# Kernel tuning notes

Hardware: AMD Instinct MI355X
Metric: run time of the kernel (lower is better)

## Reference

```python
import jax, jax.numpy as jnp
import numpy as np

N = 100000      # nodes
E = 1000000     # edges
H_DIM = 124     # node embedding dim
CLS_DIM = 4     # node class-logit dim (H_DIM + CLS_DIM = in_features = 128)
POLAR_DIM = 2   # edge_pred_features
HIDDEN = 256
OUT = 2
LN_EPS = 1e-5


def setup_inputs() -> dict:
    key = jax.random.key(0)
    ks = jax.random.split(key, 10)
    in_dim = 2 * (H_DIM + CLS_DIM) + POLAR_DIM  # 258
    return {
        "h": jax.random.normal(ks[0], (N, H_DIM), dtype=jnp.float32),
        "cls": jax.random.normal(ks[1], (N, CLS_DIM), dtype=jnp.float32),
        "polar": jax.random.normal(ks[2], (E, POLAR_DIM), dtype=jnp.float32),
        "src": jax.random.randint(ks[3], (E,), 0, N, dtype=jnp.int64),
        "dst": jax.random.randint(ks[4], (E,), 0, N, dtype=jnp.int64),
        # parameters (PyTorch Linear default-ish init scale)
        "W1": jax.random.normal(ks[5], (in_dim, HIDDEN), dtype=jnp.float32) * (1.0 / np.sqrt(in_dim)),
        "b1": jnp.zeros((HIDDEN,), dtype=jnp.float32),
        "gamma": jnp.ones((HIDDEN,), dtype=jnp.float32),
        "beta": jnp.zeros((HIDDEN,), dtype=jnp.float32),
        "W2": jax.random.normal(ks[6], (HIDDEN, OUT), dtype=jnp.float32) * (1.0 / np.sqrt(HIDDEN)),
        "b2": jnp.zeros((OUT,), dtype=jnp.float32),
    }


def reference(h, cls, polar, src, dst, W1, b1, gamma, beta, W2, b2):
    # softmax over class logits per node (same math as softmax on gathered
    # edge copies, but computed once per node)
    cls_sm = jax.nn.softmax(cls, axis=1)                  # [N, CLS_DIM]
    # gather src/dst node features along edges
    x = jnp.concatenate(
        [h[src], cls_sm[src], polar, h[dst], cls_sm[dst]], axis=1
    )                                                     # [E, 258]
    z = x @ W1 + b1                                        # [E, HIDDEN]
    # LayerNorm
    mu = jnp.mean(z, axis=-1, keepdims=True)
    var = jnp.mean(jnp.square(z - mu), axis=-1, keepdims=True)
    z = (z - mu) * jax.lax.rsqrt(var + LN_EPS) * gamma + beta
    z = jax.nn.relu(z)
    # dropout is identity in eval mode
    score = z @ W2 + b2                                    # [E, OUT]
    return score
```

## Files before the change

### kernel.cpp

```cpp
#include <hip/hip_runtime.h>
#include <hip/hip_bf16.h>

#define NN 100000
#define EE 1000000
#define H_DIM 124
#define PCOLS 512
#define LDK 136
#define CW 132

typedef float f32x4 __attribute__((ext_vector_type(4)));
typedef short bf16x8 __attribute__((ext_vector_type(8)));
typedef _Float16 h2 __attribute__((ext_vector_type(2)));

__device__ __forceinline__ unsigned short f2bf(float f) {
    unsigned int x = __float_as_uint(f);
    unsigned int r = (x + 0x7FFFu + ((x >> 16) & 1u)) >> 16;
    return (unsigned short)r;
}
__device__ __forceinline__ unsigned int pk2bf(float a, float b) {
    return (unsigned int)f2bf(a) | ((unsigned int)f2bf(b) << 16);
}
__device__ __forceinline__ unsigned int pk2h(float a, float b) {
    h2 v = (h2){(_Float16)a, (_Float16)b};
    return __builtin_bit_cast(unsigned int, v);
}

__device__ __forceinline__ float fdot2(h2 a, h2 b, float c) {
#if __has_builtin(__builtin_amdgcn_fdot2)
    return __builtin_amdgcn_fdot2(a, b, c, false);
#else
    return c + (float)a[0] * (float)b[0] + (float)a[1] * (float)b[1];
#endif
}

#if __has_builtin(__builtin_amdgcn_update_dpp)
template <int CTRL>
__device__ __forceinline__ float dpp_add(float x) {
    int xi = __builtin_bit_cast(int, x);
    int t = __builtin_amdgcn_update_dpp(xi, xi, CTRL, 0xF, 0xF, false);
    return x + __builtin_bit_cast(float, t);
}
__device__ __forceinline__ float reduce16(float x) {
    x = dpp_add<0x128>(x);
    x = dpp_add<0x124>(x);
    x = dpp_add<0x122>(x);
    x = dpp_add<0x121>(x);
    return x;
}
#else
__device__ __forceinline__ float reduce16(float x) {
    x += __shfl_xor(x, 8); x += __shfl_xor(x, 4);
    x += __shfl_xor(x, 2); x += __shfl_xor(x, 1);
    return x;
}
#endif

struct alignas(16) H8 { h2 p[4]; };

__global__ __launch_bounds__(256) void build_w1t_ct(const float* __restrict__ W1,
                                                    const float* __restrict__ gamma,
                                                    const float* __restrict__ beta,
                                                    const float* __restrict__ W2,
                                                    unsigned short* __restrict__ W1T,
                                                    uint4* __restrict__ CT) {
    if (blockIdx.x < 256) {
        int t2 = blockIdx.x * 256 + threadIdx.x;
        int j = t2 >> 7, k = t2 & 127;
        int row = (j < 256) ? k : (130 + k);
        int col = (j < 256) ? j : (j - 256);
        W1T[t2] = f2bf(W1[row * 256 + col]);
    } else {
        int t = threadIdx.x;
        if (t < 192) {
            int slot = t % 12, il = t / 12;
            int a = slot >> 1, k = slot & 1;
            int j0 = il * 16 + k * 8;
            float v[8];
            #pragma unroll
            for (int i = 0; i < 8; ++i) {
                int j = j0 + i;
                v[i] = (a == 0) ? W1[128 * 256 + j]
                     : (a == 1) ? W1[129 * 256 + j]
                     : (a == 2) ? gamma[j]
                     : (a == 3) ? beta[j]
                     : (a == 4) ? W2[2 * j]
                     :            W2[2 * j + 1];
            }
            CT[t] = make_uint4(pk2h(v[0], v[1]), pk2h(v[2], v[3]),
                               pk2h(v[4], v[5]), pk2h(v[6], v[7]));
        }
    }
}

__global__ __launch_bounds__(256) void p_gemm(const float* __restrict__ h,
                                              const float* __restrict__ cls,
                                              const unsigned short* __restrict__ W1T,
                                              const float* __restrict__ b1,
                                              _Float16* __restrict__ P) {
    __shared__ alignas(16) unsigned short As[64 * LDK];
    __shared__ alignas(16) unsigned short Bs[128 * LDK];
    float* Cs = (float*)&Bs[0];
    const int m0 = blockIdx.x * 64;
    const int t = threadIdx.x;

    #pragma unroll
    for (int it = 0; it < 4; ++it) {
        int chunk = t + it * 256;
        int r = chunk >> 4, c8 = chunk & 15;
        int row = m0 + r;
        unsigned int w0 = 0, w1 = 0, w2 = 0, w3 = 0;
        if (row < NN) {
            if (c8 < 15) {
                const float* hp = h + (size_t)row * H_DIM + c8 * 8;
                float4 v0 = *(const float4*)(hp);
                float4 v1 = *(const float4*)(hp + 4);
                w0 = pk2bf(v0.x, v0.y); w1 = pk2bf(v0.z, v0.w);
                w2 = pk2bf(v1.x, v1.y); w3 = pk2bf(v1.z, v1.w);
            } else {
                float4 v0 = *(const float4*)(h + (size_t)row * H_DIM + 120);
                float4 c = *(const float4*)(cls + (size_t)row * 4);
                float m = fmaxf(fmaxf(c.x, c.y), fmaxf(c.z, c.w));
                float e0 = __expf(c.x - m), e1 = __expf(c.y - m);
                float e2 = __expf(c.z - m), e3 = __expf(c.w - m);
                float inv = 1.0f / (e0 + e1 + e2 + e3);
                w0 = pk2bf(v0.x, v0.y); w1 = pk2bf(v0.z, v0.w);
                w2 = pk2bf(e0 * inv, e1 * inv); w3 = pk2bf(e2 * inv, e3 * inv);
            }
        }
        *(uint4*)(&As[r * LDK + c8 * 8]) = make_uint4(w0, w1, w2, w3);
    }
    __syncthreads();

    const int wave = t >> 6, lane = t & 63;
    const int wm = wave & 1, wn = wave >> 1;
    const int lm = lane & 15, quad = lane >> 4;

    bf16x8 afrag[4][2];
    #pragma unroll
    for (int s = 0; s < 4; ++s) {
        int k0 = s * 32 + quad * 8;
        #pragma unroll
        for (int mt = 0; mt < 2; ++mt)
            afrag[s][mt] = *(const bf16x8*)(&As[(wm * 32 + mt * 16 + lm) * LDK + k0]);
    }

    for (int cchunk = 0; cchunk < 4; ++cchunk) {
        const int n0 = cchunk * 128;
        if (cchunk) __syncthreads();
        #pragma unroll
        for (int it = 0; it < 8; ++it) {
            int chunk = t + it * 256;
            int r = chunk >> 4, c = chunk & 15;
            float4 v = *(const float4*)(W1T + (n0 + r) * 128 + c * 8);
            *(float4*)(&Bs[r * LDK + c * 8]) = v;
        }
        __syncthreads();

        f32x4 acc[2][4];
        #pragma unroll
        for (int mt = 0; mt < 2; ++mt)
            #pragma unroll
            for (int nt = 0; nt < 4; ++nt)
                acc[mt][nt] = (f32x4){0.f, 0.f, 0.f, 0.f};

        #pragma unroll
        for (int s = 0; s < 4; ++s) {
            int k0 = s * 32 + quad * 8;
            bf16x8 b[4];
            #pragma unroll
            for (int nt = 0; nt < 4; ++nt)
                b[nt] = *(const bf16x8*)(&Bs[(wn * 64 + nt * 16 + lm) * LDK + k0]);
            #pragma unroll
            for (int mt = 0; mt < 2; ++mt)
                #pragma unroll
                for (int nt = 0; nt < 4; ++nt)
                    acc[mt][nt] = __builtin_amdgcn_mfma_f32_16x16x32_bf16(afrag[s][mt], b[nt], acc[mt][nt], 0, 0, 0);
        }
        __syncthreads();

        #pragma unroll
        for (int mt = 0; mt < 2; ++mt)
            #pragma unroll
            for (int nt = 0; nt < 4; ++nt) {
                int col = wn * 64 + nt * 16 + lm;
                int rb  = wm * 32 + mt * 16 + quad * 4;
                #pragma unroll
                for (int r = 0; r < 4; ++r)
                    Cs[(rb + r) * CW + col] = acc[mt][nt][r];
            }
        __syncthreads();

        #pragma unroll
        for (int it = 0; it < 4; ++it) {
            int chunk = t + it * 256;
            int r = chunk >> 4, c8 = chunk & 15;
            float4 a = *(const float4*)(Cs + r * CW + c8 * 8);
            float4 b = *(const float4*)(Cs + r * CW + c8 * 8 + 4);
            if (n0 >= 256) {
                int cb = n0 + c8 * 8 - 256;
                float4 ba = *(const float4*)(b1 + cb);
                float4 bb = *(const float4*)(b1 + cb + 4);
                a.x += ba.x; a.y += ba.y; a.z += ba.z; a.w += ba.w;
                b.x += bb.x; b.y += bb.y; b.z += bb.z; b.w += bb.w;
            }
            uint4 o = make_uint4(pk2h(a.x, a.y), pk2h(a.z, a.w),
                                 pk2h(b.x, b.y), pk2h(b.z, b.w));
            int row = m0 + r;
            if (row < NN)
                *(uint4*)(P + (size_t)row * PCOLS + n0 + c8 * 8) = o;
        }
    }
}

#define K3_BLOCKS 4096
#define K3_WAVES  (K3_BLOCKS * 4)
#define K3_STRIDE (K3_WAVES * 4)
#define K3_ROUNDS 16

struct EIdx { int s, d; float q0, q1; };

__global__ __launch_bounds__(256) void edge_kernel(const _Float16* __restrict__ P,
                                                   const int* __restrict__ src,
                                                   const int* __restrict__ dst,
                                                   const float* __restrict__ polar,
                                                   const uint4* __restrict__ CT,
                                                   const float* __restrict__ b2,
                                                   float* __restrict__ out) {
    const int lane = threadIdx.x & 63;
    const int il   = lane & 15;
    const int g    = lane >> 4;
    const int wid  = blockIdx.x * 4 + (threadIdx.x >> 6);
    const char* Pb = (const char*)P;
    const int e0 = wid * 4 + g;

    uint4 cq[12];
    #pragma unroll
    for (int i = 0; i < 12; ++i) cq[i] = CT[il * 12 + i];
    h2 w0c[8], w1c[8], gc[8], bc[8], w2ac[8], w2bc[8];
    {
        const h2* ch = (const h2*)cq;
        #pragma unroll
        for (int p = 0; p < 8; ++p) {
            w0c[p]  = ch[p];      w1c[p]  = ch[8 + p];
            gc[p]   = ch[16 + p]; bc[p]   = ch[24 + p];
            w2ac[p] = ch[32 + p]; w2bc[p] = ch[40 + p];
        }
    }
    const float b20 = b2[0], b21 = b2[1];
    const h2 onep  = (h2){(_Float16)1.0f, (_Float16)1.0f};
    const h2 zerop = (h2){(_Float16)0.0f, (_Float16)0.0f};

    const unsigned boff_s = (unsigned)(il * 32);
    const unsigned boff_d = (unsigned)(512 + il * 32);

    EIdx I[4];
    H8 buf[3][4];

    #define LOAD_IDX(slot, r)                                                  \
    {                                                                          \
        int eg = e0 + (r) * K3_STRIDE;                                         \
        int ec = (eg < EE) ? eg : 0;                                           \
        I[slot].s = src[ec]; I[slot].d = dst[ec];                              \
        float2 q = *(const float2*)(polar + 2 * ec);                           \
        I[slot].q0 = q.x; I[slot].q1 = q.y;                                    \
    }

    #define LOAD_P(bslot, islot)                                               \
    {                                                                          \
        unsigned os = (unsigned)I[islot].s * 1024u + boff_s;                   \
        unsigned od = (unsigned)I[islot].d * 1024u + boff_d;                   \
        buf[bslot][0] = *(const H8*)(Pb + os);                                 \
        buf[bslot][1] = *(const H8*)(Pb + os + 16);                            \
        buf[bslot][2] = *(const H8*)(Pb + od);                                 \
        buf[bslot][3] = *(const H8*)(Pb + od + 16);                            \
    }

    LOAD_IDX(0, 0) LOAD_IDX(1, 1) LOAD_IDX(2, 2) LOAD_IDX(3, 3)
    LOAD_P(0, 0) LOAD_P(1, 1) LOAD_P(2, 2)

    #define EDGE_COMPUTE(Abuf, q0v, q1v, eg)                                   \
    {                                                                          \
        h2 p0 = (h2){(_Float16)(q0v), (_Float16)(q0v)};                        \
        h2 p1 = (h2){(_Float16)(q1v), (_Float16)(q1v)};                        \
        h2 z[8];                                                               \
        float sum = 0.f, ss = 0.f;                                             \
        _Pragma("unroll")                                                      \
        for (int p = 0; p < 8; ++p) {                                          \
            h2 pv = ((p < 4) ? (Abuf)[0].p[p] : (Abuf)[1].p[p - 4])            \
                  + ((p < 4) ? (Abuf)[2].p[p] : (Abuf)[3].p[p - 4]);           \
            h2 c = w0c[p] * p0 + w1c[p] * p1;                                  \
            z[p] = pv + c;                                                     \
            sum = fdot2(z[p], onep, sum);                                      \
            ss  = fdot2(z[p], z[p], ss);                                       \
        }                                                                      \
        sum = reduce16(sum); ss = reduce16(ss);                                \
        float mu   = sum * (1.0f / 256.0f);                                    \
        float var  = ss * (1.0f / 256.0f) - mu * mu;                           \
        float rstd = rsqrtf(var + 1e-5f);                                      \
        float nmur = -mu * rstd;                                               \
        h2 rsh  = (h2){(_Float16)rstd, (_Float16)rstd};                        \
        h2 nmh  = (h2){(_Float16)nmur, (_Float16)nmur};                        \
        float o0 = 0.f, o1 = 0.f;                                              \
        _Pragma("unroll")                                                      \
        for (int p = 0; p < 8; ++p) {                                          \
            h2 tt = z[p] * rsh + nmh;                                          \
            h2 u = tt * gc[p] + bc[p];                                         \
            u = __builtin_elementwise_max(u, zerop);                           \
            o0 = fdot2(u, w2ac[p], o0);                                        \
            o1 = fdot2(u, w2bc[p], o1);                                        \
        }                                                                      \
        o0 = reduce16(o0); o1 = reduce16(o1);                                  \
        if (il == 0 && (eg) < EE)                                              \
            *(float2*)(out + 2 * (eg)) = make_float2(o0 + b20, o1 + b21);      \
    }

    #pragma unroll
    for (int r = 0; r < K3_ROUNDS; ++r) {
        const int bi = r % 3, ii = r % 4;
        EDGE_COMPUTE(buf[bi], I[ii].q0, I[ii].q1, e0 + r * K3_STRIDE);
        if (r + 4 < K3_ROUNDS) {
            LOAD_IDX(ii, r + 4)
        }
        if (r + 3 < K3_ROUNDS) {
            LOAD_P(bi, (r + 3) % 4)
        }
    }
    #undef EDGE_COMPUTE
    #undef LOAD_P
    #undef LOAD_IDX
}

extern "C" void kernel_launch(void* const* d_in, const int* in_sizes, int n_in,
                              void* d_out, int out_size, void* d_ws, size_t ws_size,
                              hipStream_t stream) {
    const float* h     = (const float*)d_in[0];
    const float* cls   = (const float*)d_in[1];
    const float* polar = (const float*)d_in[2];
    const int*   src   = (const int*)d_in[3];
    const int*   dst   = (const int*)d_in[4];
    const float* W1    = (const float*)d_in[5];
    const float* b1    = (const float*)d_in[6];
    const float* gamma = (const float*)d_in[7];
    const float* beta  = (const float*)d_in[8];
    const float* W2    = (const float*)d_in[9];
    const float* b2    = (const float*)d_in[10];
    float* out = (float*)d_out;

    char* ws = (char*)d_ws;
    _Float16*       P   = (_Float16*)ws;
    unsigned short* W1T = (unsigned short*)(ws + 102400000);
    uint4*          CT  = (uint4*)(ws + 102531072);

    build_w1t_ct<<<257, 256, 0, stream>>>(W1, gamma, beta, W2, W1T, CT);
    p_gemm<<<1563, 256, 0, stream>>>(h, cls, W1T, b1, P);
    edge_kernel<<<K3_BLOCKS, 256, 0, stream>>>(P, src, dst, polar, CT, b2, out);
}
```

Baseline: 288.1 us.

## Deepen edge gather pipeline to four buffers and split index/polar prefetch

The edge kernel now keeps four P-row gather buffers in flight instead of three, and prefetches src/dst indices eight rounds ahead. The polar loads get their own prefetch slot. The round loop becomes a rolled outer loop over a 4-way unrolled inner body with fixed buffer slots, and the bounds guard is kept only on the final round. The LayerNorm sum is reworked so the mean no longer goes through a dot with ones. This trades more VGPR pressure and some redundant clamped loads past the last round for more memory-level parallelism on the random gathers.

After: 288.0 us. About the same (-0.0%).

```diff
diff --git a/kernel.cpp b/kernel.cpp
--- a/kernel.cpp
+++ b/kernel.cpp
@@ -217,8 +217,6 @@
 #define K3_STRIDE (K3_WAVES * 4)
 #define K3_ROUNDS 16
 
-struct EIdx { int s, d; float q0, q1; };
-
 __global__ __launch_bounds__(256) void edge_kernel(const _Float16* __restrict__ P,
                                                    const int* __restrict__ src,
                                                    const int* __restrict__ dst,
@@ -247,50 +245,55 @@
         }
     }
     const float b20 = b2[0], b21 = b2[1];
-    const h2 onep  = (h2){(_Float16)1.0f, (_Float16)1.0f};
     const h2 zerop = (h2){(_Float16)0.0f, (_Float16)0.0f};
 
     const unsigned boff_s = (unsigned)(il * 32);
     const unsigned boff_d = (unsigned)(512 + il * 32);
 
-    EIdx I[4];
-    H8 buf[3][4];
+    int   Is[4], Id[4];
+    float q[4][2];
+    H8 buf[4][4];
 
     #define LOAD_IDX(slot, r)                                                  \
     {                                                                          \
         int eg = e0 + (r) * K3_STRIDE;                                         \
         int ec = (eg < EE) ? eg : 0;                                           \
-        I[slot].s = src[ec]; I[slot].d = dst[ec];                              \
-        float2 q = *(const float2*)(polar + 2 * ec);                           \
-        I[slot].q0 = q.x; I[slot].q1 = q.y;                                    \
-    }
-
-    #define LOAD_P(bslot, islot)                                               \
+        Is[slot] = src[ec]; Id[slot] = dst[ec];                                \
+    }
+    #define LOAD_Q(slot, r)                                                    \
     {                                                                          \
-        unsigned os = (unsigned)I[islot].s * 1024u + boff_s;                   \
-        unsigned od = (unsigned)I[islot].d * 1024u + boff_d;                   \
-        buf[bslot][0] = *(const H8*)(Pb + os);                                 \
-        buf[bslot][1] = *(const H8*)(Pb + os + 16);                            \
-        buf[bslot][2] = *(const H8*)(Pb + od);                                 \
-        buf[bslot][3] = *(const H8*)(Pb + od + 16);                            \
+        int eg = e0 + (r) * K3_STRIDE;                                         \
+        int ec = (eg < EE) ? eg : 0;                                           \
+        float2 qq = *(const float2*)(polar + 2 * ec);                          \
+        q[slot][0] = qq.x; q[slot][1] = qq.y;                                  \
+    }
+    #define LOAD_P(slot)                                                       \
+    {                                                                          \
+        unsigned os = (unsigned)Is[slot] * 1024u + boff_s;                     \
+        unsigned od = (unsigned)Id[slot] * 1024u + boff_d;                     \
+        buf[slot][0] = *(const H8*)(Pb + os);                                  \
+        buf[slot][1] = *(const H8*)(Pb + os + 16);                             \
+        buf[slot][2] = *(const H8*)(Pb + od);                                  \
+        buf[slot][3] = *(const H8*)(Pb + od + 16);                             \
     }
 
     LOAD_IDX(0, 0) LOAD_IDX(1, 1) LOAD_IDX(2, 2) LOAD_IDX(3, 3)
-    LOAD_P(0, 0) LOAD_P(1, 1) LOAD_P(2, 2)
-
-    #define EDGE_COMPUTE(Abuf, q0v, q1v, eg)                                   \
+    LOAD_Q(0, 0) LOAD_Q(1, 1) LOAD_Q(2, 2) LOAD_Q(3, 3)
+    LOAD_P(0) LOAD_P(1) LOAD_P(2) LOAD_P(3)
+    LOAD_IDX(0, 4) LOAD_IDX(1, 5) LOAD_IDX(2, 6) LOAD_IDX(3, 7)
+
+    #define EDGE_COMPUTE(slot, eg, GUARD)                                      \
     {                                                                          \
-        h2 p0 = (h2){(_Float16)(q0v), (_Float16)(q0v)};                        \
-        h2 p1 = (h2){(_Float16)(q1v), (_Float16)(q1v)};                        \
+        h2 p0 = (h2){(_Float16)q[slot][0], (_Float16)q[slot][0]};              \
+        h2 p1 = (h2){(_Float16)q[slot][1], (_Float16)q[slot][1]};              \
         h2 z[8];                                                               \
         float sum = 0.f, ss = 0.f;                                             \
         _Pragma("unroll")                                                      \
         for (int p = 0; p < 8; ++p) {                                          \
-            h2 pv = ((p < 4) ? (Abuf)[0].p[p] : (Abuf)[1].p[p - 4])            \
-                  + ((p < 4) ? (Abuf)[2].p[p] : (Abuf)[3].p[p - 4]);           \
-            h2 c = w0c[p] * p0 + w1c[p] * p1;                                  \
-            z[p] = pv + c;                                                     \
-            sum = fdot2(z[p], onep, sum);                                      \
+            h2 pv = ((p < 4) ? buf[slot][0].p[p] : buf[slot][1].p[p - 4])      \
+                  + ((p < 4) ? buf[slot][2].p[p] : buf[slot][3].p[p - 4]);     \
+            z[p] = w0c[p] * p0 + (w1c[p] * p1 + pv);                           \
+            sum += (float)z[p][0] + (float)z[p][1];                            \
             ss  = fdot2(z[p], z[p], ss);                                       \
         }                                                                      \
         sum = reduce16(sum); ss = reduce16(ss);                                \
@@ -310,23 +313,28 @@
             o1 = fdot2(u, w2bc[p], o1);                                        \
         }                                                                      \
         o0 = reduce16(o0); o1 = reduce16(o1);                                  \
-        if (il == 0 && (eg) < EE)                                              \
+        if (il == 0 && (!(GUARD) || (eg) < EE))                                \
             *(float2*)(out + 2 * (eg)) = make_float2(o0 + b20, o1 + b21);      \
     }
 
-    #pragma unroll
-    for (int r = 0; r < K3_ROUNDS; ++r) {
-        const int bi = r % 3, ii = r % 4;
-        EDGE_COMPUTE(buf[bi], I[ii].q0, I[ii].q1, e0 + r * K3_STRIDE);
-        if (r + 4 < K3_ROUNDS) {
-            LOAD_IDX(ii, r + 4)
-        }
-        if (r + 3 < K3_ROUNDS) {
-            LOAD_P(bi, (r + 3) % 4)
+    for (int rr = 0; rr < 4; ++rr) {
+        int rb = rr * 4;
+        #pragma unroll
+        for (int u = 0; u < 4; ++u) {
+            int eg = e0 + (rb + u) * K3_STRIDE;
+            if (rb + u == 15) {
+                EDGE_COMPUTE(u, eg, 1)
+            } else {
+                EDGE_COMPUTE(u, eg, 0)
+            }
+            LOAD_Q(u, rb + u + 4)
+            LOAD_P(u)
+            LOAD_IDX(u, rb + u + 8)
         }
     }
     #undef EDGE_COMPUTE
     #undef LOAD_P
+    #undef LOAD_Q
     #undef LOAD_IDX
 }
 
```
